# Optimization experiments

Measured on AMD Instinct MI355X. Metric: run time of the kernel, lower is better.

## Reference

```python
import jax, jax.numpy as jnp
import numpy as np

B, N, DIM, HEADS, DHEAD, DEPTH, EDGE = 1, 384, 128, 4, 64, 3, 8
INNER = HEADS * DHEAD  # 256


def _make_rotary():
    inv = 1.0 / (10000.0 ** (np.arange(0, DHEAD, 2, dtype=np.float32) / DHEAD))
    f = np.arange(N, dtype=np.float32)[:, None] * inv[None, :]  # [N, DHEAD//2]
    f = np.repeat(f, 2, axis=-1)  # interleaved pairs -> [N, DHEAD]
    return jnp.asarray(np.cos(f)), jnp.asarray(np.sin(f))

COS, SIN = _make_rotary()


def _rotate_half(x):
    x2 = x.reshape(x.shape[:-1] + (DHEAD // 2, 2))
    return jnp.stack((-x2[..., 1], x2[..., 0]), axis=-1).reshape(x.shape)


def _layer_norm(x, s, b, eps=1e-3):
    mu = jnp.mean(x, axis=-1, keepdims=True)
    var = jnp.mean(jnp.square(x - mu), axis=-1, keepdims=True)
    return (x - mu) * jax.lax.rsqrt(var + eps) * s + b


def _gated_res(x, res, Wg):
    gi = jnp.concatenate([x, res, x - res], axis=-1)  # [B,N,3*DIM]
    g = jax.nn.sigmoid(gi @ Wg)  # [B,N,1]
    return x * g + res * (1.0 - g)


def setup_inputs() -> dict:
    key = jax.random.key(0)
    ks = jax.random.split(key, 16)
    p = lambda k, shape: 0.02 * jax.random.normal(k, shape, jnp.float32)
    return {
        "nodes": jax.random.normal(ks[0], (B, N, DIM), jnp.float32),
        "edges": jax.random.normal(ks[1], (B, N, N, EDGE), jnp.float32),
        "ln1_s": jnp.ones((DEPTH, DIM), jnp.float32), "ln1_b": jnp.zeros((DEPTH, DIM), jnp.float32),
        "Wq": p(ks[2], (DEPTH, DIM, INNER)), "bq": jnp.zeros((DEPTH, INNER), jnp.float32),
        "Wkv": p(ks[3], (DEPTH, DIM, 2 * INNER)), "bkv": jnp.zeros((DEPTH, 2 * INNER), jnp.float32),
        "We": p(ks[4], (DEPTH, EDGE, INNER)), "be": jnp.zeros((DEPTH, INNER), jnp.float32),
        "Wo": p(ks[5], (DEPTH, INNER, DIM)), "bo": jnp.zeros((DEPTH, DIM), jnp.float32),
        "Wg_attn": p(ks[6], (DEPTH, 3 * DIM, 1)),
        "ln2_s": jnp.ones((DEPTH, DIM), jnp.float32), "ln2_b": jnp.zeros((DEPTH, DIM), jnp.float32),
        "W1": p(ks[7], (DEPTH, DIM, 4 * DIM)), "b1": jnp.zeros((DEPTH, 4 * DIM), jnp.float32),
        "W2": p(ks[8], (DEPTH, 4 * DIM, DIM)), "b2": jnp.zeros((DEPTH, DIM), jnp.float32),
        "Wg_ff": p(ks[9], (DEPTH, 3 * DIM, 1)),
        "Wd1": p(ks[10], (DIM, 9)), "bd1": jnp.zeros((9,), jnp.float32),
        "Wd2": p(ks[11], (9, 3)), "bd2": jnp.zeros((3,), jnp.float32),
        "mask": jnp.ones((B, N), dtype=bool),
    }


def _forward(nodes, edges, ln1_s, ln1_b, Wq, bq, Wkv, bkv, We, be, Wo, bo, Wg_attn,
             ln2_s, ln2_b, W1, b1, W2, b2, Wg_ff, Wd1, bd1, Wd2, bd2, mask):
    cos = COS[None, None]  # [1,1,N,DHEAD]
    sin = SIN[None, None]
    mask2 = mask[:, None, :, None] & mask[:, None, None, :]  # [B,1,N,N]
    x = nodes
    for i in range(DEPTH):
        # --- pre-norm attention with edge-conditioned K/V and rotary pos emb ---
        xn = _layer_norm(x, ln1_s[i], ln1_b[i])
        q = (xn @ Wq[i] + bq[i]).reshape(B, N, HEADS, DHEAD).transpose(0, 2, 1, 3)
        k, v = jnp.split(xn @ Wkv[i] + bkv[i], 2, axis=-1)
        k = k.reshape(B, N, HEADS, DHEAD).transpose(0, 2, 1, 3)
        v = v.reshape(B, N, HEADS, DHEAD).transpose(0, 2, 1, 3)
        e = (edges @ We[i] + be[i]).reshape(B, N, N, HEADS, DHEAD).transpose(0, 3, 1, 2, 4)  # [B,H,i,j,d]
        q = q * cos + _rotate_half(q) * sin
        k = k * cos + _rotate_half(k) * sin
        kf = k[:, :, None, :, :] + e  # [B,H,i,j,d]
        vf = v[:, :, None, :, :] + e
        sim = jnp.einsum('bhid,bhijd->bhij', q, kf) * (DHEAD ** -0.5)
        sim = jnp.where(mask2, sim, -1e9)
        attn = jax.nn.softmax(sim, axis=-1)
        out = jnp.einsum('bhij,bhijd->bhid', attn, vf)
        out = out.transpose(0, 2, 1, 3).reshape(B, N, INNER) @ Wo[i] + bo[i]
        x = _gated_res(out, x, Wg_attn[i])
        # --- pre-norm feedforward ---
        xn2 = _layer_norm(x, ln2_s[i], ln2_b[i])
        h = jax.nn.gelu(xn2 @ W1[i] + b1[i], approximate=False)
        ff = h @ W2[i] + b2[i]
        x = _gated_res(ff, x, Wg_ff[i])
    y = jax.nn.relu(x @ Wd1 + bd1)
    y = y @ Wd2 + bd2  # [B,N,3]
    return y - jnp.mean(y, axis=1)  # broadcasts since B == 1 (matches TF semantics)


def reference(nodes, edges, ln1_s, ln1_b, Wq, bq, Wkv, bkv, We, be, Wo, bo, Wg_attn,
              ln2_s, ln2_b, W1, b1, W2, b2, Wg_ff, Wd1, bd1, Wd2, bd2, mask):
    return _forward(nodes, edges, ln1_s, ln1_b, Wq, bq, Wkv, bkv, We, be, Wo, bo, Wg_attn,
                    ln2_s, ln2_b, W1, b1, W2, b2, Wg_ff, Wd1, bd1, Wd2, bd2, mask)
```

## Files before the change

kernel.cpp:

```cpp
#include <hip/hip_runtime.h>
#include <math.h>

#define NTOK 384
#define DIM  128
#define HEADS 4
#define DHEAD 64
#define INNER 256
#define DEPTH 3
#define EDGE 8
#define FFD 512

__device__ __forceinline__ float wave_sum64(float v){
#pragma unroll
  for (int m = 32; m >= 1; m >>= 1) v += __shfl_xor(v, m, 64);
  return v;
}
__device__ __forceinline__ float wave_max64(float v){
#pragma unroll
  for (int m = 32; m >= 1; m >>= 1) v = fmaxf(v, __shfl_xor(v, m, 64));
  return v;
}

__device__ __forceinline__ int swz_row(int id){ return (id & 7) * 48 + (id >> 3); }

__device__ __forceinline__ void rotary_val(int i, int d, float* c, float* s){
  int j = d >> 1;
  double ex = (double)(2 * j) / 64.0;
  float p = (float)pow(10000.0, ex);
  float inv = 1.0f / p;
  float f = (float)i * inv;
  double fd = (double)f;
  *c = (float)cos(fd);
  *s = (float)sin(fd);
}

__device__ __forceinline__ void qkv_row_v2(
    int i, int t, const float* __restrict__ snx,
    const float* __restrict__ Wq, const float* __restrict__ bq,
    const float* __restrict__ Wkv, const float* __restrict__ bkv,
    const float* __restrict__ We, const float* __restrict__ be,
    const float* __restrict__ cosRow, const float* __restrict__ sinRow,
    float* __restrict__ qb_, float* __restrict__ kbT, float* __restrict__ vb_,
    float* __restrict__ qWeB, float* __restrict__ qbeB,
    float4* __restrict__ qp4)
{
  int ks   = (t < 192) ? 0 : 1;
  int quad = (t < 192) ? t : t - 192;
  float4 acc = {0.f, 0.f, 0.f, 0.f};
  if (t < 384){
    const float4* Wp; int stride4;
    if (quad < 64){ Wp = (const float4*)Wq + quad;        stride4 = 64;  }
    else          { Wp = (const float4*)Wkv + (quad - 64); stride4 = 128; }
    int k0 = ks * 64;
#pragma unroll 8
    for (int kk = 0; kk < 64; ++kk){
      int k = k0 + kk;
      float4 w = Wp[(size_t)k * stride4];
      float x = snx[k];
      acc.x = fmaf(x, w.x, acc.x); acc.y = fmaf(x, w.y, acc.y);
      acc.z = fmaf(x, w.z, acc.z); acc.w = fmaf(x, w.w, acc.w);
    }
    if (ks == 1) qp4[quad] = acc;
  }
  __syncthreads();
  if (t < 192){
    float4 p = qp4[quad];
    acc.x += p.x; acc.y += p.y; acc.z += p.z; acc.w += p.w;
    if (quad < 64){
      int c0 = 4 * quad;
      float4 b = ((const float4*)bq)[quad];
      float a0 = acc.x + b.x, a1 = acc.y + b.y, a2 = acc.z + b.z, a3 = acc.w + b.w;
      int d0 = c0 & 63;
      float c_0 = cosRow[d0],     s_0 = sinRow[d0];
      float c_1 = cosRow[d0 + 2], s_1 = sinRow[d0 + 2];
      float r0 = a0 * c_0 - a1 * s_0;
      float r1 = a1 * c_0 + a0 * s_0;
      float r2 = a2 * c_1 - a3 * s_1;
      float r3 = a3 * c_1 + a2 * s_1;
      float4 qv; qv.x = r0; qv.y = r1; qv.z = r2; qv.w = r3;
      *(float4*)(qb_ + (size_t)i * 256 + c0) = qv;
      int h = quad >> 4;
#pragma unroll
      for (int cc = 0; cc < 8; ++cc){
        const float* wc = We + cc * 256 + c0;
        float pr = r0 * wc[0] + r1 * wc[1] + r2 * wc[2] + r3 * wc[3];
#pragma unroll
        for (int m = 8; m >= 1; m >>= 1) pr += __shfl_xor(pr, m, 16);
        if ((t & 15) == 0) qWeB[(h * NTOK + i) * 8 + cc] = pr;
      }
      const float* bc = be + c0;
      float pb = r0 * bc[0] + r1 * bc[1] + r2 * bc[2] + r3 * bc[3];
#pragma unroll
      for (int m = 8; m >= 1; m >>= 1) pb += __shfl_xor(pb, m, 16);
      if ((t & 15) == 0) qbeB[h * NTOK + i] = pb;
    } else if (quad < 128){
      int c0 = 4 * (quad - 64);
      float4 b = ((const float4*)bkv)[quad - 64];
      float a0 = acc.x + b.x, a1 = acc.y + b.y, a2 = acc.z + b.z, a3 = acc.w + b.w;
      int d0 = c0 & 63, h = c0 >> 6;
      float c_0 = cosRow[d0],     s_0 = sinRow[d0];
      float c_1 = cosRow[d0 + 2], s_1 = sinRow[d0 + 2];
      float r0 = a0 * c_0 - a1 * s_0;
      float r1 = a1 * c_0 + a0 * s_0;
      float r2 = a2 * c_1 - a3 * s_1;
      float r3 = a3 * c_1 + a2 * s_1;
      float* kp = kbT + (size_t)(h * 64 + d0) * NTOK + i;
      kp[0]        = r0;
      kp[NTOK]     = r1;
      kp[2 * NTOK] = r2;
      kp[3 * NTOK] = r3;
    } else {
      int vq = quad - 128;
      int c0 = 4 * vq;
      float4 b = ((const float4*)bkv)[64 + vq];
      float4 vv;
      vv.x = acc.x + b.x; vv.y = acc.y + b.y;
      vv.z = acc.z + b.z; vv.w = acc.w + b.w;
      *(float4*)(vb_ + (size_t)i * 256 + c0) = vv;
    }
  }
}

__global__ __launch_bounds__(512) void k_lnqkv(
    const float* __restrict__ x,
    const float* __restrict__ ls, const float* __restrict__ lb,
    const float* __restrict__ Wq, const float* __restrict__ bq,
    const float* __restrict__ Wkv, const float* __restrict__ bkv,
    const float* __restrict__ We, const float* __restrict__ be,
    float* __restrict__ cosS, float* __restrict__ sinS,
    float* __restrict__ qb_, float* __restrict__ kbT, float* __restrict__ vb_,
    float* __restrict__ qWeB, float* __restrict__ qbeB)
{
  __shared__ float snx[128];
  __shared__ float crow[64], srow[64];
  __shared__ float red[4];
  __shared__ float4 qp4[192];
  int i = swz_row(blockIdx.x);
  int t = threadIdx.x;

  if (t >= 448){
    int d = t - 448;
    float c, s;
    rotary_val(i, d, &c, &s);
    crow[d] = c; srow[d] = s;
    cosS[i * 64 + d] = c; sinS[i * 64 + d] = s;
  }
  float xv = (t < 128) ? x[(size_t)i * 128 + t] : 0.f;
  float s = (t < 128) ? wave_sum64(xv) : 0.f;
  if (t == 0)  red[0] = s;
  if (t == 64) red[1] = s;
  __syncthreads();
  float mu = (red[0] + red[1]) * (1.0f / 128.0f);
  float d = xv - mu;
  float s2 = (t < 128) ? wave_sum64(d * d) : 0.f;
  if (t == 0)  red[2] = s2;
  if (t == 64) red[3] = s2;
  __syncthreads();
  if (t < 128){
    float var = (red[2] + red[3]) * (1.0f / 128.0f);
    float rstd = 1.0f / sqrtf(var + 1e-3f);
    snx[t] = d * rstd * ls[t] + lb[t];
  }
  __syncthreads();
  qkv_row_v2(i, t, snx, Wq, bq, Wkv, bkv, We, be, crow, srow,
             qb_, kbT, vb_, qWeB, qbeB, qp4);
}

__global__ __launch_bounds__(384) void k_attn(
    const float* __restrict__ qb_, const float* __restrict__ kbT, const float* __restrict__ vb_,
    const float* __restrict__ qWeB, const float* __restrict__ qbeB,
    const float* __restrict__ edges,
    const float* __restrict__ We, const float* __restrict__ be,
    float* __restrict__ aout)
{
  __shared__ float qs[64];
  __shared__ float qw[8];
  __shared__ float qbs_s;
  __shared__ float attnL[NTOK];
  __shared__ float redA[6], redB[6];
  __shared__ float red8[6][8];
  __shared__ float aws[8];
  __shared__ float part[NTOK];

  int id = blockIdx.x;
  int xcd = id & 7, loc = id >> 3;
  int i = xcd * 48 + (loc % 48);
  int h = loc / 48;
  int t = threadIdx.x, lane = t & 63, wv = t >> 6;

  if (t < 64) qs[t] = qb_[i * 256 + h * 64 + t];
  else if (t < 72) qw[t - 64] = qWeB[(h * NTOK + i) * 8 + (t - 64)];
  else if (t == 72) qbs_s = qbeB[h * NTOK + i];
  __syncthreads();

  const float* kTp = kbT + (size_t)(h * 64) * NTOK + t;
  float ac0 = 0.f, ac1 = 0.f, ac2 = 0.f, ac3 = 0.f;
#pragma unroll 8
  for (int d = 0; d < 64; d += 4){
    ac0 = fmaf(qs[d],     kTp[(size_t)d * NTOK],       ac0);
    ac1 = fmaf(qs[d + 1], kTp[(size_t)(d + 1) * NTOK], ac1);
    ac2 = fmaf(qs[d + 2], kTp[(size_t)(d + 2) * NTOK], ac2);
    ac3 = fmaf(qs[d + 3], kTp[(size_t)(d + 3) * NTOK], ac3);
  }
  const float* ep = edges + ((size_t)i * NTOK + t) * 8;
  float4 e0 = *(const float4*)ep;
  float4 e1 = *(const float4*)(ep + 4);
  float ed = e0.x * qw[0] + e0.y * qw[1] + e0.z * qw[2] + e0.w * qw[3]
           + e1.x * qw[4] + e1.y * qw[5] + e1.z * qw[6] + e1.w * qw[7];
  float sim = 0.125f * (ac0 + ac1 + ac2 + ac3 + ed + qbs_s);

  float mx = wave_max64(sim);
  if (lane == 0) redA[wv] = mx;
  __syncthreads();
  float gm = fmaxf(fmaxf(fmaxf(redA[0], redA[1]), fmaxf(redA[2], redA[3])),
                   fmaxf(redA[4], redA[5]));
  float e = expf(sim - gm);
  float sm = wave_sum64(e);
  if (lane == 0) redB[wv] = sm;
  __syncthreads();
  float tot = redB[0] + redB[1] + redB[2] + redB[3] + redB[4] + redB[5];
  float w = e / tot;
  attnL[t] = w;

  float a8[8] = { w * e0.x, w * e0.y, w * e0.z, w * e0.w,
                  w * e1.x, w * e1.y, w * e1.z, w * e1.w };
#pragma unroll
  for (int cc = 0; cc < 8; ++cc){
    float r = wave_sum64(a8[cc]);
    if (lane == 0) red8[wv][cc] = r;
  }
  __syncthreads();
  if (t < 8){
    float sa = 0.f;
#pragma unroll
    for (int g = 0; g < 6; ++g) sa += red8[g][t];
    aws[t] = sa;
  }
  __syncthreads();

  {
    int dd = lane;
    const float* vp = vb_ + h * 64 + dd;
    int j0 = wv * 64;
    float va = 0.f, vb2 = 0.f;
#pragma unroll 8
    for (int jj = 0; jj < 64; jj += 2){
      va  = fmaf(attnL[j0 + jj],     vp[(size_t)(j0 + jj) * 256],     va);
      vb2 = fmaf(attnL[j0 + jj + 1], vp[(size_t)(j0 + jj + 1) * 256], vb2);
    }
    part[t] = va + vb2;
  }
  __syncthreads();
  if (t < 64){
    float o = part[t] + part[64 + t] + part[128 + t] + part[192 + t]
            + part[256 + t] + part[320 + t];
    float ew = 0.f;
#pragma unroll
    for (int cc = 0; cc < 8; ++cc) ew = fmaf(aws[cc], We[cc * 256 + h * 64 + t], ew);
    o += ew + be[h * 64 + t];
    aout[i * 256 + h * 64 + t] = o;
  }
}

__global__ __launch_bounds__(512) void k_tail(
    const float* __restrict__ aout,
    const float* __restrict__ Wo, const float* __restrict__ bo,
    const float* __restrict__ Wg_a,
    const float* __restrict__ ln2s, const float* __restrict__ ln2b,
    const float* __restrict__ W1, const float* __restrict__ b1,
    const float* __restrict__ W2, const float* __restrict__ b2,
    const float* __restrict__ Wg_f,
    const float* __restrict__ xin, float* __restrict__ xout,
    int has_next,
    const float* __restrict__ ls_n, const float* __restrict__ lb_n,
    const float* __restrict__ Wq_n, const float* __restrict__ bq_n,
    const float* __restrict__ Wkv_n, const float* __restrict__ bkv_n,
    const float* __restrict__ We_n, const float* __restrict__ be_n,
    const float* __restrict__ cosS, const float* __restrict__ sinS,
    float* __restrict__ qb_, float* __restrict__ kbT, float* __restrict__ vb_,
    float* __restrict__ qWeB, float* __restrict__ qbeB)
{
  __shared__ float ar[256];
  __shared__ float xold[128];
  __shared__ float xrow[128];
  __shared__ float snx[128];
  __shared__ float hs[512];
  __shared__ float4 prL[512];
  __shared__ float red[4];
  float* prF = (float*)prL;

  int i = swz_row(blockIdx.x);
  int t = threadIdx.x;

  if (t < 64)            ((float4*)ar)[t]        = ((const float4*)(aout + (size_t)i * 256))[t];
  else if (t < 96)       ((float4*)xold)[t - 64] = ((const float4*)(xin + (size_t)i * 128))[t - 64];
  __syncthreads();

  {
    int colq = t & 31, ksub = t >> 5;
    const float4* Wo4 = (const float4*)Wo;
    float4 acc = {0.f, 0.f, 0.f, 0.f};
#pragma unroll
    for (int kk = 0; kk < 16; ++kk){
      int k = ksub * 16 + kk;
      float4 w = Wo4[(size_t)k * 32 + colq];
      float a = ar[k];
      acc.x = fmaf(a, w.x, acc.x); acc.y = fmaf(a, w.y, acc.y);
      acc.z = fmaf(a, w.z, acc.z); acc.w = fmaf(a, w.w, acc.w);
    }
    prL[ksub * 32 + colq] = acc;
  }
  __syncthreads();

  float o = 0.f;
  if (t < 128){
    o = bo[t];
#pragma unroll
    for (int s = 0; s < 16; ++s) o += prF[s * 128 + t];
    float xo = xold[t];
    float gp = o * Wg_a[t] + xo * Wg_a[128 + t] + (o - xo) * Wg_a[256 + t];
    float sg = wave_sum64(gp);
    if (t == 0)  red[0] = sg;
    if (t == 64) red[1] = sg;
  }
  __syncthreads();
  if (t < 128){
    float z = red[0] + red[1];
    float gg = 1.0f / (1.0f + expf(-z));
    xrow[t] = o * gg + xold[t] * (1.0f - gg);
  }
  __syncthreads();
  float xv2 = (t < 128) ? xrow[t] : 0.f;
  float s = (t < 128) ? wave_sum64(xv2) : 0.f;
  if (t == 0)  red[0] = s;
  if (t == 64) red[1] = s;
  __syncthreads();
  float mu = (red[0] + red[1]) * (1.0f / 128.0f);
  float dcen = xv2 - mu;
  float s2 = (t < 128) ? wave_sum64(dcen * dcen) : 0.f;
  if (t == 0)  red[2] = s2;
  if (t == 64) red[3] = s2;
  __syncthreads();
  if (t < 128){
    float var = (red[2] + red[3]) * (1.0f / 128.0f);
    float rstd = 1.0f / sqrtf(var + 1e-3f);
    snx[t] = dcen * rstd * ln2s[t] + ln2b[t];
  }
  __syncthreads();

  {
    int colq = t & 127, ksub = t >> 7;
    const float4* W14 = (const float4*)W1;
    float4 acc = {0.f, 0.f, 0.f, 0.f};
#pragma unroll 8
    for (int kk = 0; kk < 32; ++kk){
      int k = ksub * 32 + kk;
      float4 w = W14[(size_t)k * 128 + colq];
      float a = snx[k];
      acc.x = fmaf(a, w.x, acc.x); acc.y = fmaf(a, w.y, acc.y);
      acc.z = fmaf(a, w.z, acc.z); acc.w = fmaf(a, w.w, acc.w);
    }
    prL[ksub * 128 + colq] = acc;
  }
  __syncthreads();

  {
    float h = b1[t];
#pragma unroll
    for (int s3 = 0; s3 < 4; ++s3) h += prF[s3 * 512 + t];
    const float RS2 = 0.70710678118654752440f;
    hs[t] = 0.5f * h * (1.0f + erff(h * RS2));
  }
  __syncthreads();

  {
    int colq = t & 31, ksub = t >> 5;
    const float4* W24 = (const float4*)W2;
    float4 acc = {0.f, 0.f, 0.f, 0.f};
#pragma unroll 8
    for (int kk = 0; kk < 32; ++kk){
      int k = ksub * 32 + kk;
      float4 w = W24[(size_t)k * 32 + colq];
      float a = hs[k];
      acc.x = fmaf(a, w.x, acc.x); acc.y = fmaf(a, w.y, acc.y);
      acc.z = fmaf(a, w.z, acc.z); acc.w = fmaf(a, w.w, acc.w);
    }
    prL[ksub * 32 + colq] = acc;
  }
  __syncthreads();

  float f = 0.f;
  if (t < 128){
    f = b2[t];
#pragma unroll
    for (int s3 = 0; s3 < 16; ++s3) f += prF[s3 * 128 + t];
    float xr = xrow[t];
    float gp = f * Wg_f[t] + xr * Wg_f[128 + t] + (f - xr) * Wg_f[256 + t];
    float sg = wave_sum64(gp);
    if (t == 0)  red[0] = sg;
    if (t == 64) red[1] = sg;
  }
  __syncthreads();
  float xnew = 0.f;
  if (t < 128){
    float z = red[0] + red[1];
    float gg = 1.0f / (1.0f + expf(-z));
    xnew = f * gg + xrow[t] * (1.0f - gg);
    xout[(size_t)i * 128 + t] = xnew;
  }
  if (has_next){
    float sn = (t < 128) ? wave_sum64(xnew) : 0.f;
    if (t == 0)  red[0] = sn;
    if (t == 64) red[1] = sn;
    __syncthreads();
    float mun = (red[0] + red[1]) * (1.0f / 128.0f);
    float dn = xnew - mun;
    float sn2 = (t < 128) ? wave_sum64(dn * dn) : 0.f;
    if (t == 0)  red[2] = sn2;
    if (t == 64) red[3] = sn2;
    __syncthreads();
    if (t < 128){
      float var = (red[2] + red[3]) * (1.0f / 128.0f);
      float rstd = 1.0f / sqrtf(var + 1e-3f);
      snx[t] = dn * rstd * ls_n[t] + lb_n[t];
    }
    __syncthreads();
    qkv_row_v2(i, t, snx, Wq_n, bq_n, Wkv_n, bkv_n, We_n, be_n,
               cosS + (size_t)i * 64, sinS + (size_t)i * 64,
               qb_, kbT, vb_, qWeB, qbeB, prL);
  }
}

__global__ __launch_bounds__(384) void k_final(
    const float* __restrict__ x,
    const float* __restrict__ Wd1, const float* __restrict__ bd1,
    const float* __restrict__ Wd2, const float* __restrict__ bd2,
    float* __restrict__ out)
{
  __shared__ float red[6];
  int i = threadIdx.x;
  float y[9];
#pragma unroll
  for (int c = 0; c < 9; ++c) y[c] = bd1[c];
  const float4* x4 = (const float4*)(x + (size_t)i * 128);
#pragma unroll 8
  for (int r4 = 0; r4 < 32; ++r4){
    float4 xv = x4[r4];
    const float* wp = Wd1 + (r4 * 4) * 9;
#pragma unroll
    for (int c = 0; c < 9; ++c) y[c] = fmaf(xv.x, wp[c], y[c]);
#pragma unroll
    for (int c = 0; c < 9; ++c) y[c] = fmaf(xv.y, wp[9 + c], y[c]);
#pragma unroll
    for (int c = 0; c < 9; ++c) y[c] = fmaf(xv.z, wp[18 + c], y[c]);
#pragma unroll
    for (int c = 0; c < 9; ++c) y[c] = fmaf(xv.w, wp[27 + c], y[c]);
  }
#pragma unroll
  for (int c = 0; c < 9; ++c) y[c] = fmaxf(y[c], 0.0f);
  float z[3];
#pragma unroll
  for (int c = 0; c < 3; ++c){
    float a = bd2[c];
#pragma unroll
    for (int r = 0; r < 9; ++r) a = fmaf(y[r], Wd2[r * 3 + c], a);
    z[c] = a;
  }
#pragma unroll
  for (int c = 0; c < 3; ++c){
    float s = wave_sum64(z[c]);
    if ((i & 63) == 0) red[i >> 6] = s;
    __syncthreads();
    float tot = 0.f;
#pragma unroll
    for (int w = 0; w < 6; ++w) tot += red[w];
    float mean = tot * (1.0f / 384.0f);
    out[i * 3 + c] = z[c] - mean;
    __syncthreads();
  }
}

extern "C" void kernel_launch(void* const* d_in, const int* in_sizes, int n_in,
                              void* d_out, int out_size, void* d_ws, size_t ws_size,
                              hipStream_t stream)
{
  const float* nodes   = (const float*)d_in[0];
  const float* edges   = (const float*)d_in[1];
  const float* ln1_s   = (const float*)d_in[2];
  const float* ln1_b   = (const float*)d_in[3];
  const float* Wq      = (const float*)d_in[4];
  const float* bq      = (const float*)d_in[5];
  const float* Wkv     = (const float*)d_in[6];
  const float* bkv     = (const float*)d_in[7];
  const float* We      = (const float*)d_in[8];
  const float* be      = (const float*)d_in[9];
  const float* Wo      = (const float*)d_in[10];
  const float* bo      = (const float*)d_in[11];
  const float* Wg_attn = (const float*)d_in[12];
  const float* ln2_s   = (const float*)d_in[13];
  const float* ln2_b   = (const float*)d_in[14];
  const float* W1      = (const float*)d_in[15];
  const float* b1      = (const float*)d_in[16];
  const float* W2      = (const float*)d_in[17];
  const float* b2      = (const float*)d_in[18];
  const float* Wg_ff   = (const float*)d_in[19];
  const float* Wd1     = (const float*)d_in[20];
  const float* bd1     = (const float*)d_in[21];
  const float* Wd2     = (const float*)d_in[22];
  const float* bd2     = (const float*)d_in[23];

  float* ws   = (float*)d_ws;
  float* cosS = ws;
  float* sinS = cosS + 24576;
  float* qbuf = sinS + 24576;
  float* kbT  = qbuf + 98304;
  float* vbuf = kbT + 98304;
  float* qWeB = vbuf + 98304;
  float* qbeB = qWeB + 12288;
  float* aoutB = qbeB + 1536;
  float* xbuf = aoutB + 98304;

  k_lnqkv<<<dim3(NTOK), dim3(512), 0, stream>>>(
      nodes, ln1_s, ln1_b, Wq, bq, Wkv, bkv, We, be,
      cosS, sinS, qbuf, kbT, vbuf, qWeB, qbeB);

  for (int L = 0; L < DEPTH; ++L){
    int Ln = (L < DEPTH - 1) ? (L + 1) : L;
    k_attn<<<dim3(NTOK * HEADS), dim3(384), 0, stream>>>(
        qbuf, kbT, vbuf, qWeB, qbeB, edges,
        We + (size_t)L * EDGE * INNER, be + L * INNER, aoutB);
    k_tail<<<dim3(NTOK), dim3(512), 0, stream>>>(
        aoutB, Wo + (size_t)L * INNER * DIM, bo + L * DIM,
        Wg_attn + L * 3 * DIM,
        ln2_s + L * DIM, ln2_b + L * DIM,
        W1 + (size_t)L * DIM * FFD, b1 + L * FFD,
        W2 + (size_t)L * FFD * DIM, b2 + L * DIM,
        Wg_ff + L * 3 * DIM,
        (L == 0) ? nodes : xbuf, xbuf,
        (L < DEPTH - 1) ? 1 : 0,
        ln1_s + Ln * DIM, ln1_b + Ln * DIM,
        Wq + (size_t)Ln * DIM * INNER, bq + Ln * INNER,
        Wkv + (size_t)Ln * DIM * 2 * INNER, bkv + Ln * 2 * INNER,
        We + (size_t)Ln * EDGE * INNER, be + Ln * INNER,
        cosS, sinS, qbuf, kbT, vbuf, qWeB, qbeB);
  }

  k_final<<<dim3(1), dim3(384), 0, stream>>>(xbuf, Wd1, bd1, Wd2, bd2, (float*)d_out);
}
```

Baseline: 138.0 us.

## Fuse attention into per-row layer kernel with ping-pong QKV buffers

Merges the per-(row,head) attention kernel into the per-row tail kernel. One 512-thread block now computes all four heads' attention, the output projection, FFN, gating and the next layer's QKV. QKV buffers are double-buffered so a layer can write the next layer's Q/K/V while other blocks still read the current ones. Layer norms and gating reductions are reduced to a single wave each, which removes several block barriers. This drops one launch per layer and the aout round trip through global memory, in exchange for 384 blocks instead of 1536 for the attention phase.

```diff
diff --git a/kernel.cpp b/kernel.cpp
--- a/kernel.cpp
+++ b/kernel.cpp
@@ -49,7 +49,7 @@
   float4 acc = {0.f, 0.f, 0.f, 0.f};
   if (t < 384){
     const float4* Wp; int stride4;
-    if (quad < 64){ Wp = (const float4*)Wq + quad;        stride4 = 64;  }
+    if (quad < 64){ Wp = (const float4*)Wq + quad;         stride4 = 64;  }
     else          { Wp = (const float4*)Wkv + (quad - 64); stride4 = 128; }
     int k0 = ks * 64;
 #pragma unroll 8
@@ -133,7 +133,6 @@
 {
   __shared__ float snx[128];
   __shared__ float crow[64], srow[64];
-  __shared__ float red[4];
   __shared__ float4 qp4[192];
   int i = swz_row(blockIdx.x);
   int t = threadIdx.x;
@@ -145,125 +144,25 @@
     crow[d] = c; srow[d] = s;
     cosS[i * 64 + d] = c; sinS[i * 64 + d] = s;
   }
-  float xv = (t < 128) ? x[(size_t)i * 128 + t] : 0.f;
-  float s = (t < 128) ? wave_sum64(xv) : 0.f;
-  if (t == 0)  red[0] = s;
-  if (t == 64) red[1] = s;
-  __syncthreads();
-  float mu = (red[0] + red[1]) * (1.0f / 128.0f);
-  float d = xv - mu;
-  float s2 = (t < 128) ? wave_sum64(d * d) : 0.f;
-  if (t == 0)  red[2] = s2;
-  if (t == 64) red[3] = s2;
-  __syncthreads();
-  if (t < 128){
-    float var = (red[2] + red[3]) * (1.0f / 128.0f);
+  if (t < 64){
+    float x0 = x[(size_t)i * 128 + t], x1 = x[(size_t)i * 128 + 64 + t];
+    float mu = wave_sum64(x0 + x1) * (1.0f / 128.0f);
+    float d0 = x0 - mu, d1 = x1 - mu;
+    float var = wave_sum64(d0 * d0 + d1 * d1) * (1.0f / 128.0f);
     float rstd = 1.0f / sqrtf(var + 1e-3f);
-    snx[t] = d * rstd * ls[t] + lb[t];
+    snx[t]      = d0 * rstd * ls[t]      + lb[t];
+    snx[t + 64] = d1 * rstd * ls[t + 64] + lb[t + 64];
   }
   __syncthreads();
   qkv_row_v2(i, t, snx, Wq, bq, Wkv, bkv, We, be, crow, srow,
              qb_, kbT, vb_, qWeB, qbeB, qp4);
 }
 
-__global__ __launch_bounds__(384) void k_attn(
+__global__ __launch_bounds__(512) void k_layer(
     const float* __restrict__ qb_, const float* __restrict__ kbT, const float* __restrict__ vb_,
     const float* __restrict__ qWeB, const float* __restrict__ qbeB,
     const float* __restrict__ edges,
     const float* __restrict__ We, const float* __restrict__ be,
-    float* __restrict__ aout)
-{
-  __shared__ float qs[64];
-  __shared__ float qw[8];
-  __shared__ float qbs_s;
-  __shared__ float attnL[NTOK];
-  __shared__ float redA[6], redB[6];
-  __shared__ float red8[6][8];
-  __shared__ float aws[8];
-  __shared__ float part[NTOK];
-
-  int id = blockIdx.x;
-  int xcd = id & 7, loc = id >> 3;
-  int i = xcd * 48 + (loc % 48);
-  int h = loc / 48;
-  int t = threadIdx.x, lane = t & 63, wv = t >> 6;
-
-  if (t < 64) qs[t] = qb_[i * 256 + h * 64 + t];
-  else if (t < 72) qw[t - 64] = qWeB[(h * NTOK + i) * 8 + (t - 64)];
-  else if (t == 72) qbs_s = qbeB[h * NTOK + i];
-  __syncthreads();
-
-  const float* kTp = kbT + (size_t)(h * 64) * NTOK + t;
-  float ac0 = 0.f, ac1 = 0.f, ac2 = 0.f, ac3 = 0.f;
-#pragma unroll 8
-  for (int d = 0; d < 64; d += 4){
-    ac0 = fmaf(qs[d],     kTp[(size_t)d * NTOK],       ac0);
-    ac1 = fmaf(qs[d + 1], kTp[(size_t)(d + 1) * NTOK], ac1);
-    ac2 = fmaf(qs[d + 2], kTp[(size_t)(d + 2) * NTOK], ac2);
-    ac3 = fmaf(qs[d + 3], kTp[(size_t)(d + 3) * NTOK], ac3);
-  }
-  const float* ep = edges + ((size_t)i * NTOK + t) * 8;
-  float4 e0 = *(const float4*)ep;
-  float4 e1 = *(const float4*)(ep + 4);
-  float ed = e0.x * qw[0] + e0.y * qw[1] + e0.z * qw[2] + e0.w * qw[3]
-           + e1.x * qw[4] + e1.y * qw[5] + e1.z * qw[6] + e1.w * qw[7];
-  float sim = 0.125f * (ac0 + ac1 + ac2 + ac3 + ed + qbs_s);
-
-  float mx = wave_max64(sim);
-  if (lane == 0) redA[wv] = mx;
-  __syncthreads();
-  float gm = fmaxf(fmaxf(fmaxf(redA[0], redA[1]), fmaxf(redA[2], redA[3])),
-                   fmaxf(redA[4], redA[5]));
-  float e = expf(sim - gm);
-  float sm = wave_sum64(e);
-  if (lane == 0) redB[wv] = sm;
-  __syncthreads();
-  float tot = redB[0] + redB[1] + redB[2] + redB[3] + redB[4] + redB[5];
-  float w = e / tot;
-  attnL[t] = w;
-
-  float a8[8] = { w * e0.x, w * e0.y, w * e0.z, w * e0.w,
-                  w * e1.x, w * e1.y, w * e1.z, w * e1.w };
-#pragma unroll
-  for (int cc = 0; cc < 8; ++cc){
-    float r = wave_sum64(a8[cc]);
-    if (lane == 0) red8[wv][cc] = r;
-  }
-  __syncthreads();
-  if (t < 8){
-    float sa = 0.f;
-#pragma unroll
-    for (int g = 0; g < 6; ++g) sa += red8[g][t];
-    aws[t] = sa;
-  }
-  __syncthreads();
-
-  {
-    int dd = lane;
-    const float* vp = vb_ + h * 64 + dd;
-    int j0 = wv * 64;
-    float va = 0.f, vb2 = 0.f;
-#pragma unroll 8
-    for (int jj = 0; jj < 64; jj += 2){
-      va  = fmaf(attnL[j0 + jj],     vp[(size_t)(j0 + jj) * 256],     va);
-      vb2 = fmaf(attnL[j0 + jj + 1], vp[(size_t)(j0 + jj + 1) * 256], vb2);
-    }
-    part[t] = va + vb2;
-  }
-  __syncthreads();
-  if (t < 64){
-    float o = part[t] + part[64 + t] + part[128 + t] + part[192 + t]
-            + part[256 + t] + part[320 + t];
-    float ew = 0.f;
-#pragma unroll
-    for (int cc = 0; cc < 8; ++cc) ew = fmaf(aws[cc], We[cc * 256 + h * 64 + t], ew);
-    o += ew + be[h * 64 + t];
-    aout[i * 256 + h * 64 + t] = o;
-  }
-}
-
-__global__ __launch_bounds__(512) void k_tail(
-    const float* __restrict__ aout,
     const float* __restrict__ Wo, const float* __restrict__ bo,
     const float* __restrict__ Wg_a,
     const float* __restrict__ ln2s, const float* __restrict__ ln2b,
@@ -277,23 +176,113 @@
     const float* __restrict__ Wkv_n, const float* __restrict__ bkv_n,
     const float* __restrict__ We_n, const float* __restrict__ be_n,
     const float* __restrict__ cosS, const float* __restrict__ sinS,
-    float* __restrict__ qb_, float* __restrict__ kbT, float* __restrict__ vb_,
-    float* __restrict__ qWeB, float* __restrict__ qbeB)
+    float* __restrict__ qb_o, float* __restrict__ kbT_o, float* __restrict__ vb_o,
+    float* __restrict__ qWeB_o, float* __restrict__ qbeB_o)
 {
+  __shared__ float qsL[256];
+  __shared__ float qw[4][8];
+  __shared__ float qbe[4];
+  __shared__ float attnL[4][384];
+  __shared__ float redA[8], redB[8];
+  __shared__ float red8[8][8];
+  __shared__ float part[512];
   __shared__ float ar[256];
   __shared__ float xold[128];
   __shared__ float xrow[128];
   __shared__ float snx[128];
   __shared__ float hs[512];
   __shared__ float4 prL[512];
-  __shared__ float red[4];
   float* prF = (float*)prL;
 
   int i = swz_row(blockIdx.x);
   int t = threadIdx.x;
 
-  if (t < 64)            ((float4*)ar)[t]        = ((const float4*)(aout + (size_t)i * 256))[t];
-  else if (t < 96)       ((float4*)xold)[t - 64] = ((const float4*)(xin + (size_t)i * 128))[t - 64];
+  if (t < 256) qsL[t] = qb_[(size_t)i * 256 + t];
+  else if (t < 288){ int idx = t - 256; qw[idx >> 3][idx & 7] = qWeB[((idx >> 3) * NTOK + i) * 8 + (idx & 7)]; }
+  else if (t < 292) qbe[t - 288] = qbeB[(t - 288) * NTOK + i];
+  else if (t >= 384) xold[t - 384] = xin[(size_t)i * 128 + (t - 384)];
+  __syncthreads();
+
+  int h = t >> 7, jj = t & 127;
+  int wv = t >> 6;
+  float sims[3];
+  float4 e0s[3], e1s[3];
+  {
+    float qbv = qbe[h];
+    const float* qsp = qsL + h * 64;
+#pragma unroll
+    for (int rep = 0; rep < 3; ++rep){
+      int j = jj + rep * 128;
+      const float* kTp = kbT + (size_t)(h * 64) * NTOK + j;
+      float a0 = 0.f, a1 = 0.f, a2 = 0.f, a3 = 0.f;
+#pragma unroll 8
+      for (int d = 0; d < 64; d += 4){
+        a0 = fmaf(qsp[d],     kTp[(size_t)d * NTOK],       a0);
+        a1 = fmaf(qsp[d + 1], kTp[(size_t)(d + 1) * NTOK], a1);
+        a2 = fmaf(qsp[d + 2], kTp[(size_t)(d + 2) * NTOK], a2);
+        a3 = fmaf(qsp[d + 3], kTp[(size_t)(d + 3) * NTOK], a3);
+      }
+      const float* ep = edges + ((size_t)i * NTOK + j) * 8;
+      float4 e0 = *(const float4*)ep;
+      float4 e1 = *(const float4*)(ep + 4);
+      e0s[rep] = e0; e1s[rep] = e1;
+      float ed = e0.x * qw[h][0] + e0.y * qw[h][1] + e0.z * qw[h][2] + e0.w * qw[h][3]
+               + e1.x * qw[h][4] + e1.y * qw[h][5] + e1.z * qw[h][6] + e1.w * qw[h][7];
+      sims[rep] = 0.125f * (a0 + a1 + a2 + a3 + ed + qbv);
+    }
+  }
+  float mx = wave_max64(fmaxf(sims[0], fmaxf(sims[1], sims[2])));
+  if ((t & 63) == 0) redA[wv] = mx;
+  __syncthreads();
+  float gm = fmaxf(redA[2 * h], redA[2 * h + 1]);
+  float ex0 = expf(sims[0] - gm), ex1 = expf(sims[1] - gm), ex2 = expf(sims[2] - gm);
+  float sm = wave_sum64(ex0 + ex1 + ex2);
+  if ((t & 63) == 0) redB[wv] = sm;
+  __syncthreads();
+  float inv = 1.0f / (redB[2 * h] + redB[2 * h + 1]);
+  float w0 = ex0 * inv, w1 = ex1 * inv, w2 = ex2 * inv;
+  attnL[h][jj] = w0; attnL[h][jj + 128] = w1; attnL[h][jj + 256] = w2;
+  {
+    float a8[8];
+    a8[0] = w0 * e0s[0].x + w1 * e0s[1].x + w2 * e0s[2].x;
+    a8[1] = w0 * e0s[0].y + w1 * e0s[1].y + w2 * e0s[2].y;
+    a8[2] = w0 * e0s[0].z + w1 * e0s[1].z + w2 * e0s[2].z;
+    a8[3] = w0 * e0s[0].w + w1 * e0s[1].w + w2 * e0s[2].w;
+    a8[4] = w0 * e1s[0].x + w1 * e1s[1].x + w2 * e1s[2].x;
+    a8[5] = w0 * e1s[0].y + w1 * e1s[1].y + w2 * e1s[2].y;
+    a8[6] = w0 * e1s[0].z + w1 * e1s[1].z + w2 * e1s[2].z;
+    a8[7] = w0 * e1s[0].w + w1 * e1s[1].w + w2 * e1s[2].w;
+#pragma unroll
+    for (int cc = 0; cc < 8; ++cc){
+      float r = wave_sum64(a8[cc]);
+      if ((t & 63) == 0) red8[wv][cc] = r;
+    }
+  }
+  __syncthreads();
+
+  {
+    int hh = t >> 7, dd = t & 63, half = (t >> 6) & 1;
+    const float* vp = vb_ + hh * 64 + dd;
+    const float* aw_ = attnL[hh];
+    int j0 = half * 192;
+    float va = 0.f, vb2 = 0.f;
+#pragma unroll 8
+    for (int jj2 = 0; jj2 < 192; jj2 += 2){
+      va  = fmaf(aw_[j0 + jj2],     vp[(size_t)(j0 + jj2) * 256],     va);
+      vb2 = fmaf(aw_[j0 + jj2 + 1], vp[(size_t)(j0 + jj2 + 1) * 256], vb2);
+    }
+    part[t] = va + vb2;
+  }
+  __syncthreads();
+  if (t < 256){
+    int h2 = t >> 6, d = t & 63;
+    float o = part[h2 * 128 + d] + part[h2 * 128 + 64 + d];
+    float ew = 0.f;
+#pragma unroll
+    for (int cc = 0; cc < 8; ++cc)
+      ew = fmaf(red8[2 * h2][cc] + red8[2 * h2 + 1][cc], We[cc * 256 + h2 * 64 + d], ew);
+    ar[t] = o + ew + be[h2 * 64 + d];
+  }
   __syncthreads();
 
   {
@@ -312,39 +301,24 @@
   }
   __syncthreads();
 
-  float o = 0.f;
-  if (t < 128){
-    o = bo[t];
-#pragma unroll
-    for (int s = 0; s < 16; ++s) o += prF[s * 128 + t];
-    float xo = xold[t];
-    float gp = o * Wg_a[t] + xo * Wg_a[128 + t] + (o - xo) * Wg_a[256 + t];
-    float sg = wave_sum64(gp);
-    if (t == 0)  red[0] = sg;
-    if (t == 64) red[1] = sg;
-  }
-  __syncthreads();
-  if (t < 128){
-    float z = red[0] + red[1];
+  if (t < 64){
+    float o0 = bo[t], o1 = bo[t + 64];
+#pragma unroll
+    for (int s = 0; s < 16; ++s){ o0 += prF[s * 128 + t]; o1 += prF[s * 128 + 64 + t]; }
+    float xo0 = xold[t], xo1 = xold[t + 64];
+    float gp = o0 * Wg_a[t]      + xo0 * Wg_a[128 + t] + (o0 - xo0) * Wg_a[256 + t]
+             + o1 * Wg_a[64 + t] + xo1 * Wg_a[192 + t] + (o1 - xo1) * Wg_a[320 + t];
+    float z = wave_sum64(gp);
     float gg = 1.0f / (1.0f + expf(-z));
-    xrow[t] = o * gg + xold[t] * (1.0f - gg);
-  }
-  __syncthreads();
-  float xv2 = (t < 128) ? xrow[t] : 0.f;
-  float s = (t < 128) ? wave_sum64(xv2) : 0.f;
-  if (t == 0)  red[0] = s;
-  if (t == 64) red[1] = s;
-  __syncthreads();
-  float mu = (red[0] + red[1]) * (1.0f / 128.0f);
-  float dcen = xv2 - mu;
-  float s2 = (t < 128) ? wave_sum64(dcen * dcen) : 0.f;
-  if (t == 0)  red[2] = s2;
-  if (t == 64) red[3] = s2;
-  __syncthreads();
-  if (t < 128){
-    float var = (red[2] + red[3]) * (1.0f / 128.0f);
+    float xr0 = o0 * gg + xo0 * (1.0f - gg);
+    float xr1 = o1 * gg + xo1 * (1.0f - gg);
+    xrow[t] = xr0; xrow[t + 64] = xr1;
+    float mu = wave_sum64(xr0 + xr1) * (1.0f / 128.0f);
+    float d0 = xr0 - mu, d1 = xr1 - mu;
+    float var = wave_sum64(d0 * d0 + d1 * d1) * (1.0f / 128.0f);
     float rstd = 1.0f / sqrtf(var + 1e-3f);
-    snx[t] = dcen * rstd * ln2s[t] + ln2b[t];
+    snx[t]      = d0 * rstd * ln2s[t]      + ln2b[t];
+    snx[t + 64] = d1 * rstd * ln2s[t + 64] + ln2b[t + 64];
   }
   __syncthreads();
 
@@ -365,11 +339,11 @@
   __syncthreads();
 
   {
-    float h = b1[t];
-#pragma unroll
-    for (int s3 = 0; s3 < 4; ++s3) h += prF[s3 * 512 + t];
+    float hv = b1[t];
+#pragma unroll
+    for (int s3 = 0; s3 < 4; ++s3) hv += prF[s3 * 512 + t];
     const float RS2 = 0.70710678118654752440f;
-    hs[t] = 0.5f * h * (1.0f + erff(h * RS2));
+    hs[t] = 0.5f * hv * (1.0f + erff(hv * RS2));
   }
   __syncthreads();
 
@@ -389,45 +363,34 @@
   }
   __syncthreads();
 
-  float f = 0.f;
-  if (t < 128){
-    f = b2[t];
-#pragma unroll
-    for (int s3 = 0; s3 < 16; ++s3) f += prF[s3 * 128 + t];
-    float xr = xrow[t];
-    float gp = f * Wg_f[t] + xr * Wg_f[128 + t] + (f - xr) * Wg_f[256 + t];
-    float sg = wave_sum64(gp);
-    if (t == 0)  red[0] = sg;
-    if (t == 64) red[1] = sg;
-  }
-  __syncthreads();
-  float xnew = 0.f;
-  if (t < 128){
-    float z = red[0] + red[1];
+  if (t < 64){
+    float f0 = b2[t], f1 = b2[t + 64];
+#pragma unroll
+    for (int s3 = 0; s3 < 16; ++s3){ f0 += prF[s3 * 128 + t]; f1 += prF[s3 * 128 + 64 + t]; }
+    float xr0 = xrow[t], xr1 = xrow[t + 64];
+    float gp = f0 * Wg_f[t]      + xr0 * Wg_f[128 + t] + (f0 - xr0) * Wg_f[256 + t]
+             + f1 * Wg_f[64 + t] + xr1 * Wg_f[192 + t] + (f1 - xr1) * Wg_f[320 + t];
+    float z = wave_sum64(gp);
     float gg = 1.0f / (1.0f + expf(-z));
-    xnew = f * gg + xrow[t] * (1.0f - gg);
-    xout[(size_t)i * 128 + t] = xnew;
-  }
+    float xn0 = f0 * gg + xr0 * (1.0f - gg);
+    float xn1 = f1 * gg + xr1 * (1.0f - gg);
+    xout[(size_t)i * 128 + t]      = xn0;
+    xout[(size_t)i * 128 + 64 + t] = xn1;
+    if (has_next){
+      float mu = wave_sum64(xn0 + xn1) * (1.0f / 128.0f);
+      float d0 = xn0 - mu, d1 = xn1 - mu;
+      float var = wave_sum64(d0 * d0 + d1 * d1) * (1.0f / 128.0f);
+      float rstd = 1.0f / sqrtf(var + 1e-3f);
+      snx[t]      = d0 * rstd * ls_n[t]      + lb_n[t];
+      snx[t + 64] = d1 * rstd * ls_n[t + 64] + lb_n[t + 64];
+    }
+  }
+  __syncthreads();
+
   if (has_next){
-    float sn = (t < 128) ? wave_sum64(xnew) : 0.f;
-    if (t == 0)  red[0] = sn;
-    if (t == 64) red[1] = sn;
-    __syncthreads();
-    float mun = (red[0] + red[1]) * (1.0f / 128.0f);
-    float dn = xnew - mun;
-    float sn2 = (t < 128) ? wave_sum64(dn * dn) : 0.f;
-    if (t == 0)  red[2] = sn2;
-    if (t == 64) red[3] = sn2;
-    __syncthreads();
-    if (t < 128){
-      float var = (red[2] + red[3]) * (1.0f / 128.0f);
-      float rstd = 1.0f / sqrtf(var + 1e-3f);
-      snx[t] = dn * rstd * ls_n[t] + lb_n[t];
-    }
-    __syncthreads();
     qkv_row_v2(i, t, snx, Wq_n, bq_n, Wkv_n, bkv_n, We_n, be_n,
                cosS + (size_t)i * 64, sinS + (size_t)i * 64,
-               qb_, kbT, vb_, qWeB, qbeB, prL);
+               qb_o, kbT_o, vb_o, qWeB_o, qbeB_o, prL);
   }
 }
 
@@ -512,25 +475,39 @@
   float* ws   = (float*)d_ws;
   float* cosS = ws;
   float* sinS = cosS + 24576;
-  float* qbuf = sinS + 24576;
-  float* kbT  = qbuf + 98304;
-  float* vbuf = kbT + 98304;
-  float* qWeB = vbuf + 98304;
-  float* qbeB = qWeB + 12288;
-  float* aoutB = qbeB + 1536;
-  float* xbuf = aoutB + 98304;
+  float* qb0   = sinS + 24576;
+  float* kbT0  = qb0 + 98304;
+  float* vb0   = kbT0 + 98304;
+  float* qWe0  = vb0 + 98304;
+  float* qbe0  = qWe0 + 12288;
+  float* qb1   = qbe0 + 1536;
+  float* kbT1  = qb1 + 98304;
+  float* vb1   = kbT1 + 98304;
+  float* qWe1  = vb1 + 98304;
+  float* qbe1  = qWe1 + 12288;
+  float* xbuf  = qbe1 + 1536;
 
   k_lnqkv<<<dim3(NTOK), dim3(512), 0, stream>>>(
       nodes, ln1_s, ln1_b, Wq, bq, Wkv, bkv, We, be,
-      cosS, sinS, qbuf, kbT, vbuf, qWeB, qbeB);
+      cosS, sinS, qb0, kbT0, vb0, qWe0, qbe0);
 
   for (int L = 0; L < DEPTH; ++L){
     int Ln = (L < DEPTH - 1) ? (L + 1) : L;
-    k_attn<<<dim3(NTOK * HEADS), dim3(384), 0, stream>>>(
-        qbuf, kbT, vbuf, qWeB, qbeB, edges,
-        We + (size_t)L * EDGE * INNER, be + L * INNER, aoutB);
-    k_tail<<<dim3(NTOK), dim3(512), 0, stream>>>(
-        aoutB, Wo + (size_t)L * INNER * DIM, bo + L * DIM,
+    const float* qbi  = (L & 1) ? qb1  : qb0;
+    const float* kbi  = (L & 1) ? kbT1 : kbT0;
+    const float* vbi  = (L & 1) ? vb1  : vb0;
+    const float* qWei = (L & 1) ? qWe1 : qWe0;
+    const float* qbei = (L & 1) ? qbe1 : qbe0;
+    float* qbo  = (L & 1) ? qb0  : qb1;
+    float* kbo  = (L & 1) ? kbT0 : kbT1;
+    float* vbo  = (L & 1) ? vb0  : vb1;
+    float* qWeo = (L & 1) ? qWe0 : qWe1;
+    float* qbeo = (L & 1) ? qbe0 : qbe1;
+
+    k_layer<<<dim3(NTOK), dim3(512), 0, stream>>>(
+        qbi, kbi, vbi, qWei, qbei, edges,
+        We + (size_t)L * EDGE * INNER, be + L * INNER,
+        Wo + (size_t)L * INNER * DIM, bo + L * DIM,
         Wg_attn + L * 3 * DIM,
         ln2_s + L * DIM, ln2_b + L * DIM,
         W1 + (size_t)L * DIM * FFD, b1 + L * FFD,
@@ -542,7 +519,7 @@
         Wq + (size_t)Ln * DIM * INNER, bq + Ln * INNER,
         Wkv + (size_t)Ln * DIM * 2 * INNER, bkv + Ln * 2 * INNER,
         We + (size_t)Ln * EDGE * INNER, be + Ln * INNER,
-        cosS, sinS, qbuf, kbT, vbuf, qWeB, qbeB);
+        cosS, sinS, qbo, kbo, vbo, qWeo, qbeo);
   }
 
   k_final<<<dim3(1), dim3(384), 0, stream>>>(xbuf, Wd1, bd1, Wd2, bd2, (float*)d_out);
```

New measurement: 135.3 us. Within noise of the previous version (-1.9%).
